# Performance work log

Measured on AMD Instinct MI355X. Metric: run time of the kernel, lower is better.

Reference implementation:

```python
import jax, jax.numpy as jnp
import numpy as np

NUM_HEADS = 16
DIM_EMBED = 1024
DIM_CROSS = 768
DIM_HEAD = DIM_EMBED // NUM_HEADS


def setup_inputs() -> dict:
    key = jax.random.key(0)
    ks = jax.random.split(key, 10)
    B, Sq, Skv = 16, 4096, 77
    s_e = 1.0 / np.sqrt(DIM_EMBED)
    s_c = 1.0 / np.sqrt(DIM_CROSS)
    return {
        "x": jax.random.normal(ks[0], (B, Sq, DIM_EMBED), jnp.float32),
        "y": jax.random.normal(ks[1], (B, Skv, DIM_CROSS), jnp.float32),
        "wq": jax.random.uniform(ks[2], (DIM_EMBED, DIM_EMBED), jnp.float32, -s_e, s_e),
        "bq": jax.random.uniform(ks[3], (DIM_EMBED,), jnp.float32, -s_e, s_e),
        "wk": jax.random.uniform(ks[4], (DIM_CROSS, DIM_EMBED), jnp.float32, -s_c, s_c),
        "bk": jax.random.uniform(ks[5], (DIM_EMBED,), jnp.float32, -s_c, s_c),
        "wv": jax.random.uniform(ks[6], (DIM_CROSS, DIM_EMBED), jnp.float32, -s_c, s_c),
        "bv": jax.random.uniform(ks[7], (DIM_EMBED,), jnp.float32, -s_c, s_c),
        "wo": jax.random.uniform(ks[8], (DIM_EMBED, DIM_EMBED), jnp.float32, -s_e, s_e),
        "bo": jax.random.uniform(ks[9], (DIM_EMBED,), jnp.float32, -s_e, s_e),
    }


def reference(x, y, wq, bq, wk, bk, wv, bv, wo, bo):
    B, Sq, E = x.shape
    H, D = NUM_HEADS, DIM_HEAD
    q = (x @ wq + bq).reshape(B, Sq, H, D).transpose(0, 2, 1, 3)   # [B,H,Sq,D]
    k = (y @ wk + bk).reshape(B, -1, H, D).transpose(0, 2, 1, 3)   # [B,H,Skv,D]
    v = (y @ wv + bv).reshape(B, -1, H, D).transpose(0, 2, 1, 3)   # [B,H,Skv,D]
    scale = 1.0 / jnp.sqrt(jnp.asarray(D, dtype=q.dtype))
    scores = jnp.einsum("bhqd,bhkd->bhqk", q, k) * scale           # [B,H,Sq,Skv]
    attn = jax.nn.softmax(scores, axis=-1)
    out = jnp.einsum("bhqk,bhkd->bhqd", attn, v)                   # [B,H,Sq,D]
    out = out.transpose(0, 2, 1, 3).reshape(B, Sq, E)
    return out @ wo + bo
```

## Files before the change

### kernel.cpp

```cpp
#include <hip/hip_runtime.h>

typedef unsigned short u16;
typedef __attribute__((ext_vector_type(4))) float f32x4;
typedef __attribute__((ext_vector_type(8))) short bf16x8;
typedef __attribute__((ext_vector_type(8))) unsigned short u16x8;
typedef __attribute__((ext_vector_type(4))) unsigned short u16x4;

__device__ __forceinline__ u16 f2bf(float f) {
  union { float f; unsigned u; } v; v.f = f;
  unsigned r = v.u + 0x7FFFu + ((v.u >> 16) & 1u);
  return (u16)(r >> 16);
}
__device__ __forceinline__ float bf2f(u16 h) {
  union { unsigned u; float f; } v; v.u = ((unsigned)h) << 16; return v.f;
}

__device__ __forceinline__ void gload_lds16(const void* g, void* l) {
  __builtin_amdgcn_global_load_lds((const __attribute__((address_space(1))) void*)g,
                                   (__attribute__((address_space(3))) void*)l, 16, 0, 0);
}


__global__ void k_zero(u16x8* __restrict__ p, int n8) {
  int i = blockIdx.x * blockDim.x + threadIdx.x;
  int stride = gridDim.x * blockDim.x;
  u16x8 z = (u16x8)0;
  for (; i < n8; i += stride) p[i] = z;
}

__global__ void k_cvt_x(const float* __restrict__ in, u16* __restrict__ out, int n4) {
  int i = blockIdx.x * blockDim.x + threadIdx.x;
  int stride = gridDim.x * blockDim.x;
  const f32x4* in4 = (const f32x4*)in;
  u16x4* out4 = (u16x4*)out;
  for (; i < n4; i += stride) {
    f32x4 v = in4[i];
    u16x4 o;
    o[0] = f2bf(v[0]); o[1] = f2bf(v[1]); o[2] = f2bf(v[2]); o[3] = f2bf(v[3]);
    out4[i] = o;
  }
}

__global__ void k_prep_wt(const float* __restrict__ wq, const float* __restrict__ wo,
                          const float* __restrict__ wk, const float* __restrict__ wv,
                          u16* __restrict__ WQ1T, u16* __restrict__ WO1T,
                          u16* __restrict__ WK1T, u16* __restrict__ WV1T) {
  __shared__ u16 tile[64][72];
  int bid = blockIdx.x;
  const float* w; u16* o; int K;
  if (bid < 256)      { w = wq; o = WQ1T; K = 1024; }
  else if (bid < 512) { w = wo; o = WO1T; K = 1024; bid -= 256; }
  else if (bid < 704) { w = wk; o = WK1T; K = 768;  bid -= 512; }
  else                { w = wv; o = WV1T; K = 768;  bid -= 704; }
  const int ti = bid >> 4, tj = bid & 15;
  const int t = threadIdx.x;
  const int r = t >> 2, cq = (t & 3) * 16;

  const float* src = w + (size_t)(ti * 64 + r) * 1024 + tj * 64 + cq;
#pragma unroll
  for (int j4 = 0; j4 < 4; ++j4) {
    f32x4 v = *(const f32x4*)(src + j4 * 4);
#pragma unroll
    for (int e = 0; e < 4; ++e) tile[r][cq + j4 * 4 + e] = f2bf(v[e]);
  }
  __syncthreads();

  u16 vals[16];
#pragma unroll
  for (int j = 0; j < 16; ++j) vals[j] = tile[cq + j][r];
  u16* dst = o + (size_t)(tj * 64 + r) * K + ti * 64 + cq;
  *(u16x8*)dst = *(u16x8*)&vals[0];
  *(u16x8*)(dst + 8) = *(u16x8*)&vals[8];
}

__global__ void k_prep_y(const float* __restrict__ y, u16* __restrict__ yb, int n4) {
  int i = blockIdx.x * blockDim.x + threadIdx.x;
  int stride = gridDim.x * blockDim.x;
  const f32x4* in4 = (const f32x4*)y;
  u16x4* out4 = (u16x4*)yb;
  for (; i < n4; i += stride) {
    f32x4 v = in4[i];
    u16x4 o;
    o[0] = f2bf(v[0]); o[1] = f2bf(v[1]); o[2] = f2bf(v[2]); o[3] = f2bf(v[3]);
    out4[i] = o;
  }
}

__global__ __launch_bounds__(256, 2) void k_gemm_kv(
    const u16* __restrict__ A,
    const u16* __restrict__ BK1, const float* __restrict__ bkb, u16* __restrict__ KTo,
    const u16* __restrict__ BV1, const float* __restrict__ bvb, u16* __restrict__ VTo)
{
  const int M = 1232, Kdim = 768;
  __shared__ u16 sA[128 * 32];
  __shared__ u16 sB[128 * 32];
  const int t = threadIdx.x;
  const int half = blockIdx.x >= 80;
  const int bb = blockIdx.x - half * 80;
  const u16* B = half ? BV1 : BK1;
  const float* bias = half ? bvb : bkb;
  u16* outp = half ? VTo : KTo;
  const int bm = bb / 8, bn = bb % 8;
  const int m0 = bm * 128, n0 = bn * 128;
  const int l = t & 63, wv_ = t >> 6;
  const int lr = l & 15, lg = l >> 4;
  const int wm = (wv_ >> 1) * 64, wn = (wv_ & 1) * 64;

  const int srow = t >> 2;
  const int ssw = ((t >> 2) & 3) ^ ((t >> 4) & 3);
  const int scol = ((t & 3) ^ ssw) * 8;
  char* ldsA = (char*)sA;
  char* ldsB = (char*)sB;
  const int ldsoff = wv_ * 1024;

  const int swl = (lr & 3) ^ ((lr >> 2) & 3);
  const int rds = (lg ^ swl) * 8;

  f32x4 acc[4][4] = {};

  for (int kt = 0; kt < Kdim / 32; ++kt) {
    const int k0 = kt * 32;
    __syncthreads();
    {
      int r1 = m0 + srow;       if (r1 > M - 1) r1 = M - 1;
      int r2 = m0 + 64 + srow;  if (r2 > M - 1) r2 = M - 1;
      gload_lds16(A + (size_t)r1 * Kdim + k0 + scol, ldsA + 0    + ldsoff);
      gload_lds16(A + (size_t)r2 * Kdim + k0 + scol, ldsA + 4096 + ldsoff);
      gload_lds16(B + (size_t)(n0 + srow) * Kdim + k0 + scol,      ldsB + 0    + ldsoff);
      gload_lds16(B + (size_t)(n0 + 64 + srow) * Kdim + k0 + scol, ldsB + 4096 + ldsoff);
    }
    __syncthreads();
    bf16x8 af[4], bfr[4];
#pragma unroll
    for (int mt = 0; mt < 4; ++mt)
      af[mt] = *(const bf16x8*)&sA[(wm + mt * 16 + lr) * 32 + rds];
#pragma unroll
    for (int nt = 0; nt < 4; ++nt)
      bfr[nt] = *(const bf16x8*)&sB[(wn + nt * 16 + lr) * 32 + rds];
#pragma unroll
    for (int mt = 0; mt < 4; ++mt)
#pragma unroll
      for (int nt = 0; nt < 4; ++nt)
        acc[mt][nt] = __builtin_amdgcn_mfma_f32_16x16x32_bf16(af[mt], bfr[nt], acc[mt][nt], 0, 0, 0);
  }

#pragma unroll
  for (int mt = 0; mt < 4; ++mt) {
#pragma unroll
    for (int nt = 0; nt < 4; ++nt) {
      const int gc = n0 + wn + nt * 16 + lr;
      const float bb2 = bias[gc];
#pragma unroll
      for (int r = 0; r < 4; ++r) {
        const int gr = m0 + wm + mt * 16 + lg * 4 + r;
        const float v = acc[mt][nt][r] + bb2;
        if (gr < M) {
          int bI = gr / 77, s = gr - bI * 77;
          int hh = gc >> 6, d = gc & 63;
          if (!half)
            outp[(((size_t)bI * 16 + hh) * 96 + s) * 64 + d] = f2bf(v);
          else
            outp[(((size_t)bI * 16 + hh) * 64 + d) * 96 + s] = f2bf(v);
        }
      }
    }
  }
}

template <int EPI>
__global__ __launch_bounds__(512, 2) void gemm8p(
    const u16* __restrict__ A, const u16* __restrict__ Bp,
    const float* __restrict__ bias, void* __restrict__ outp,
    const u16* __restrict__ KT, const u16* __restrict__ VT)
{
  __shared__ char lds[131072];
  const int t = threadIdx.x;
  const int cpx = (int)gridDim.x >> 3;
  const int swz = ((int)blockIdx.x & 7) * cpx + ((int)blockIdx.x >> 3);
  const int bm = swz >> 2, bn = swz & 3;
  const int m0 = bm * 256, n0 = bn * 256;
  const int w = t >> 6, l = t & 63, lr = l & 15, lg = l >> 4;
  const int wm = w >> 2, wn = w & 3;

  const int srow = t >> 3;
  const int scol = ((t & 7) ^ ((t >> 3) & 7)) << 3;
  const int sw0 = ((lg) ^ (lr & 7)) << 4;
  const int sw1 = ((4 + lg) ^ (lr & 7)) << 4;
  const int abase = wm * 128 + lr;
  const int bbase = wn * 64 + lr;

  f32x4 acc[8][4] = {};

#define RD_A(dst, db, mh, ksw) { _Pragma("unroll") for (int q = 0; q < 4; ++q) \
    dst[q] = *(const bf16x8*)(lds + (db) + ((abase + (mh) * 64 + q * 16) << 7) + (ksw)); }
#define RD_B(dst, db, ksw) { _Pragma("unroll") for (int nt = 0; nt < 4; ++nt) \
    dst[nt] = *(const bf16x8*)(lds + (db) + 32768 + ((bbase + nt * 16) << 7) + (ksw)); }
#define STG_A(kt, dn, j) gload_lds16(A + (size_t)(m0 + (j) * 64 + srow) * 1024 + (kt) * 64 + scol, \
                                     lds + (dn) + (j) * 8192 + t * 16)
#define STG_B(kt, dn, j) gload_lds16(Bp + (size_t)(n0 + (j) * 64 + srow) * 1024 + (kt) * 64 + scol, \
                                     lds + (dn) + 32768 + (j) * 8192 + t * 16)
#define MM16(ab, a_, b_) { __builtin_amdgcn_s_setprio(1); \
  _Pragma("unroll") for (int q = 0; q < 4; ++q) \
    _Pragma("unroll") for (int nt = 0; nt < 4; ++nt) \
      acc[(ab) + q][nt] = __builtin_amdgcn_mfma_f32_16x16x32_bf16(a_[q], b_[nt], acc[(ab) + q][nt], 0, 0, 0); \
  __builtin_amdgcn_s_setprio(0); }
#define BAR __builtin_amdgcn_s_barrier()
#define SB0 __builtin_amdgcn_sched_barrier(0)
#define VM2 asm volatile("s_waitcnt vmcnt(2)" ::: "memory")
#define VM4 asm volatile("s_waitcnt vmcnt(4)" ::: "memory")

  STG_B(0, 0, 0); STG_B(0, 0, 1);
  STG_A(0, 0, 0); STG_A(0, 0, 2);
  STG_B(0, 0, 2); STG_B(0, 0, 3);
  STG_A(0, 0, 1); STG_A(0, 0, 3);
  VM2; SB0; BAR;

#pragma unroll 2
  for (int c = 0; c < 16; ++c) {
    const int db = (c & 1) * 65536, dn = db ^ 65536;
    int cn = c + 1; if (cn > 15) cn = 15;
    bf16x8 a_[4], b0[4], b1[4];
    RD_A(a_, db, 0, sw0); RD_B(b0, db, sw0);
    STG_B(cn, dn, 0); STG_B(cn, dn, 1);
    BAR;
    MM16(0, a_, b0);
    BAR;
    RD_A(a_, db, 0, sw1); RD_B(b1, db, sw1);
    STG_A(cn, dn, 0); STG_A(cn, dn, 2);
    VM4; SB0; BAR;
    MM16(0, a_, b1);
    BAR;
    RD_A(a_, db, 1, sw0);
    STG_B(cn, dn, 2); STG_B(cn, dn, 3);
    BAR;
    MM16(4, a_, b0);
    BAR;
    RD_A(a_, db, 1, sw1);
    STG_A(cn, dn, 1); STG_A(cn, dn, 3);
    VM2; SB0; BAR;
    MM16(4, a_, b1);
    BAR;
  }
  asm volatile("s_waitcnt vmcnt(0)" ::: "memory");
  SB0; BAR;

#undef RD_A
#undef RD_B
#undef STG_A
#undef STG_B
#undef MM16
#undef BAR
#undef SB0
#undef VM2
#undef VM4

  if constexpr (EPI == 1) {
#pragma unroll
    for (int q = 0; q < 8; ++q) {
#pragma unroll
      for (int nt = 0; nt < 4; ++nt) {
        const int gc = n0 + wn * 64 + nt * 16 + lr;
        const float bb = bias[gc];
#pragma unroll
        for (int r = 0; r < 4; ++r) {
          const int gr = m0 + wm * 128 + q * 16 + lg * 4 + r;
          ((float*)outp)[(size_t)gr * 1024 + gc] = acc[q][nt][r] + bb;
        }
      }
    }
  } else {
    const int hh = (n0 >> 6) + wn;
    const int b = m0 >> 12;
    const u16* gK = KT + (size_t)(b * 16 + hh) * (96 * 64);
    const u16* gV = VT + (size_t)(b * 16 + hh) * (64 * 96);
    u16* Qs = (u16*)(lds + w * 16384);
    u16* Ps = (u16*)(lds + w * 16384 + 8192);
    u16* QBo = (u16*)outp;

    bf16x8 fk[5][2], fv[4][3];
#pragma unroll
    for (int nt = 0; nt < 5; ++nt)
#pragma unroll
      for (int ks = 0; ks < 2; ++ks)
        fk[nt][ks] = *(const bf16x8*)&gK[(nt * 16 + lr) * 64 + ks * 32 + lg * 8];
#pragma unroll
    for (int nt = 0; nt < 4; ++nt)
#pragma unroll
      for (int ks = 0; ks < 3; ++ks)
        fv[nt][ks] = *(const bf16x8*)&gV[(nt * 16 + lr) * 96 + ks * 32 + lg * 8];

    float bb[4];
#pragma unroll
    for (int nt = 0; nt < 4; ++nt) bb[nt] = bias[n0 + wn * 64 + nt * 16 + lr];

#pragma unroll
    for (int cc = 0; cc < 4; ++cc) {
#pragma unroll
      for (int qq = 0; qq < 2; ++qq)
#pragma unroll
        for (int nt = 0; nt < 4; ++nt)
#pragma unroll
          for (int r = 0; r < 4; ++r)
            Qs[(qq * 16 + lg * 4 + r) * 72 + nt * 16 + lr] =
                f2bf(acc[cc * 2 + qq][nt][r] + bb[nt]);

      bf16x8 aq[2][2];
#pragma unroll
      for (int qq = 0; qq < 2; ++qq)
#pragma unroll
        for (int ks = 0; ks < 2; ++ks)
          aq[qq][ks] = *(const bf16x8*)&Qs[(qq * 16 + lr) * 72 + ks * 32 + lg * 8];

      f32x4 s_[2][5] = {};
#pragma unroll
      for (int nt = 0; nt < 5; ++nt)
#pragma unroll
        for (int ks = 0; ks < 2; ++ks)
#pragma unroll
          for (int qq = 0; qq < 2; ++qq)
            s_[qq][nt] = __builtin_amdgcn_mfma_f32_16x16x32_bf16(aq[qq][ks], fk[nt][ks], s_[qq][nt], 0, 0, 0);
#pragma unroll
      for (int qq = 0; qq < 2; ++qq)
#pragma unroll
        for (int nt = 0; nt < 5; ++nt)
#pragma unroll
          for (int r = 0; r < 4; ++r)
            s_[qq][nt][r] *= 0.125f;
      if (lr >= 13) {
#pragma unroll
        for (int qq = 0; qq < 2; ++qq)
#pragma unroll
          for (int r = 0; r < 4; ++r)
            s_[qq][4][r] = -1e30f;
      }

      float ri[2][4];
#pragma unroll
      for (int qq = 0; qq < 2; ++qq) {
#pragma unroll
        for (int r = 0; r < 4; ++r) {
          float m1 = s_[qq][0][r];
#pragma unroll
          for (int nt = 1; nt < 5; ++nt) m1 = fmaxf(m1, s_[qq][nt][r]);
          m1 = fmaxf(m1, __shfl_xor(m1, 1, 64));
          m1 = fmaxf(m1, __shfl_xor(m1, 2, 64));
          m1 = fmaxf(m1, __shfl_xor(m1, 4, 64));
          m1 = fmaxf(m1, __shfl_xor(m1, 8, 64));
          float s1 = 0.f;
#pragma unroll
          for (int nt = 0; nt < 5; ++nt) {
            float e = __expf(s_[qq][nt][r] - m1);
            s_[qq][nt][r] = e;
            s1 += e;
          }
          s1 += __shfl_xor(s1, 1, 64);
          s1 += __shfl_xor(s1, 2, 64);
          s1 += __shfl_xor(s1, 4, 64);
          s1 += __shfl_xor(s1, 8, 64);
          ri[qq][r] = 1.0f / s1;
        }
      }

#pragma unroll
      for (int qq = 0; qq < 2; ++qq)
#pragma unroll
        for (int nt = 0; nt < 5; ++nt)
#pragma unroll
          for (int r = 0; r < 4; ++r)
            Ps[(qq * 16 + lg * 4 + r) * 104 + nt * 16 + lr] = f2bf(s_[qq][nt][r] * ri[qq][r]);
#pragma unroll
      for (int qq = 0; qq < 2; ++qq)
#pragma unroll
        for (int r = 0; r < 4; ++r)
          Ps[(qq * 16 + lg * 4 + r) * 104 + 80 + lr] = 0;

      f32x4 o_[2][4] = {};
#pragma unroll
      for (int ks = 0; ks < 3; ++ks) {
        bf16x8 ap[2];
#pragma unroll
        for (int qq = 0; qq < 2; ++qq)
          ap[qq] = *(const bf16x8*)&Ps[(qq * 16 + lr) * 104 + ks * 32 + lg * 8];
#pragma unroll
        for (int nt = 0; nt < 4; ++nt)
#pragma unroll
          for (int qq = 0; qq < 2; ++qq)
            o_[qq][nt] = __builtin_amdgcn_mfma_f32_16x16x32_bf16(ap[qq], fv[nt][ks], o_[qq][nt], 0, 0, 0);
      }

#pragma unroll
      for (int qq = 0; qq < 2; ++qq)
#pragma unroll
        for (int nt = 0; nt < 4; ++nt)
#pragma unroll
          for (int r = 0; r < 4; ++r)
            QBo[(size_t)(m0 + wm * 128 + cc * 32 + qq * 16 + lg * 4 + r) * 1024
                + hh * 64 + nt * 16 + lr] = f2bf(o_[qq][nt][r]);
    }
  }
}


extern "C" void kernel_launch(void* const* d_in, const int* in_sizes, int n_in,
                              void* d_out, int out_size, void* d_ws, size_t ws_size,
                              hipStream_t stream) {
  const float* x  = (const float*)d_in[0];
  const float* y  = (const float*)d_in[1];
  const float* wq = (const float*)d_in[2];
  const float* bq = (const float*)d_in[3];
  const float* wk = (const float*)d_in[4];
  const float* bk = (const float*)d_in[5];
  const float* wv = (const float*)d_in[6];
  const float* bv = (const float*)d_in[7];
  const float* wo = (const float*)d_in[8];
  const float* bo = (const float*)d_in[9];

  char* ws = (char*)d_ws;
  u16* QB   = (u16*)(ws + 0);
  u16* WQ1T = (u16*)(ws + 134217728);
  u16* WO1T = (u16*)(ws + 136314880);
  u16* WK1T = (u16*)(ws + 138412032);
  u16* WV1T = (u16*)(ws + 139984896);
  u16* YB   = (u16*)(ws + 141557760);
  u16* KT   = (u16*)(ws + 143654912);
  u16* VT   = (u16*)(ws + 146800640);

  u16*   XB  = (u16*)d_out;
  float* OUT = (float*)d_out;

  k_zero<<<768, 256, 0, stream>>>((u16x8*)KT, 393216);
  k_cvt_x<<<4096, 256, 0, stream>>>(x, XB, 16777216);
  k_prep_wt<<<896, 256, 0, stream>>>(wq, wo, wk, wv, WQ1T, WO1T, WK1T, WV1T);
  k_prep_y<<<924, 256, 0, stream>>>(y, YB, 236544);

  k_gemm_kv<<<160, 256, 0, stream>>>(YB, WK1T, bk, KT, WV1T, bv, VT);

  gemm8p<0><<<1024, 512, 0, stream>>>(XB, WQ1T, bq, QB, KT, VT);

  gemm8p<1><<<1024, 512, 0, stream>>>(QB, WO1T, bo, OUT, nullptr, nullptr);
}
```

Baseline: 490.3 us.

## Split output projection into dedicated kernel with 4-stage K=32 pipelined GEMM

The templated GEMM is split into two kernels: the Q-projection+attention kernel keeps the old main loop, while the output projection gets its own GEMM. The new one uses K-tiles of 32 with four LDS stages, a different XOR swizzle, and register double-buffered fragment reads. It uses s_setprio around the MFMA blocks and prefetches three stages ahead to hide global-load latency. The change is meant to improve load/compute overlap for the plain GEMM, at the cost of more barriers per K step and duplicated code.

```diff
diff --git a/kernel.cpp b/kernel.cpp
--- a/kernel.cpp
+++ b/kernel.cpp
@@ -167,10 +167,9 @@
   }
 }
 
-template <int EPI>
-__global__ __launch_bounds__(512, 2) void gemm8p(
+__global__ __launch_bounds__(512, 2) void k_qattn(
     const u16* __restrict__ A, const u16* __restrict__ Bp,
-    const float* __restrict__ bias, void* __restrict__ outp,
+    const float* __restrict__ bias, u16* __restrict__ QBo,
     const u16* __restrict__ KT, const u16* __restrict__ VT)
 {
   __shared__ char lds[131072];
@@ -254,148 +253,222 @@
 #undef VM2
 #undef VM4
 
-  if constexpr (EPI == 1) {
-#pragma unroll
-    for (int q = 0; q < 8; ++q) {
-#pragma unroll
-      for (int nt = 0; nt < 4; ++nt) {
-        const int gc = n0 + wn * 64 + nt * 16 + lr;
-        const float bb = bias[gc];
-#pragma unroll
-        for (int r = 0; r < 4; ++r) {
-          const int gr = m0 + wm * 128 + q * 16 + lg * 4 + r;
-          ((float*)outp)[(size_t)gr * 1024 + gc] = acc[q][nt][r] + bb;
+  const int hh = (n0 >> 6) + wn;
+  const int b = m0 >> 12;
+  const u16* gK = KT + (size_t)(b * 16 + hh) * (96 * 64);
+  const u16* gV = VT + (size_t)(b * 16 + hh) * (64 * 96);
+  u16* Qs = (u16*)(lds + w * 16384);
+  u16* Ps = (u16*)(lds + w * 16384 + 8192);
+
+  bf16x8 fk[5][2], fv[4][3];
+#pragma unroll
+  for (int nt = 0; nt < 5; ++nt)
+#pragma unroll
+    for (int ks = 0; ks < 2; ++ks)
+      fk[nt][ks] = *(const bf16x8*)&gK[(nt * 16 + lr) * 64 + ks * 32 + lg * 8];
+#pragma unroll
+  for (int nt = 0; nt < 4; ++nt)
+#pragma unroll
+    for (int ks = 0; ks < 3; ++ks)
+      fv[nt][ks] = *(const bf16x8*)&gV[(nt * 16 + lr) * 96 + ks * 32 + lg * 8];
+
+  float bb[4];
+#pragma unroll
+  for (int nt = 0; nt < 4; ++nt) bb[nt] = bias[n0 + wn * 64 + nt * 16 + lr];
+
+#pragma unroll
+  for (int cc = 0; cc < 4; ++cc) {
+#pragma unroll
+    for (int qq = 0; qq < 2; ++qq)
+#pragma unroll
+      for (int nt = 0; nt < 4; ++nt)
+#pragma unroll
+        for (int r = 0; r < 4; ++r)
+          Qs[(qq * 16 + lg * 4 + r) * 72 + nt * 16 + lr] =
+              f2bf(acc[cc * 2 + qq][nt][r] + bb[nt]);
+
+    bf16x8 aq[2][2];
+#pragma unroll
+    for (int qq = 0; qq < 2; ++qq)
+#pragma unroll
+      for (int ks = 0; ks < 2; ++ks)
+        aq[qq][ks] = *(const bf16x8*)&Qs[(qq * 16 + lr) * 72 + ks * 32 + lg * 8];
+
+    f32x4 s_[2][5] = {};
+#pragma unroll
+    for (int nt = 0; nt < 5; ++nt)
+#pragma unroll
+      for (int ks = 0; ks < 2; ++ks)
+#pragma unroll
+        for (int qq = 0; qq < 2; ++qq)
+          s_[qq][nt] = __builtin_amdgcn_mfma_f32_16x16x32_bf16(aq[qq][ks], fk[nt][ks], s_[qq][nt], 0, 0, 0);
+#pragma unroll
+    for (int qq = 0; qq < 2; ++qq)
+#pragma unroll
+      for (int nt = 0; nt < 5; ++nt)
+#pragma unroll
+        for (int r = 0; r < 4; ++r)
+          s_[qq][nt][r] *= 0.125f;
+    if (lr >= 13) {
+#pragma unroll
+      for (int qq = 0; qq < 2; ++qq)
+#pragma unroll
+        for (int r = 0; r < 4; ++r)
+          s_[qq][4][r] = -1e30f;
+    }
+
+    float ri[2][4];
+#pragma unroll
+    for (int qq = 0; qq < 2; ++qq) {
+#pragma unroll
+      for (int r = 0; r < 4; ++r) {
+        float m1 = s_[qq][0][r];
+#pragma unroll
+        for (int nt = 1; nt < 5; ++nt) m1 = fmaxf(m1, s_[qq][nt][r]);
+        m1 = fmaxf(m1, __shfl_xor(m1, 1, 64));
+        m1 = fmaxf(m1, __shfl_xor(m1, 2, 64));
+        m1 = fmaxf(m1, __shfl_xor(m1, 4, 64));
+        m1 = fmaxf(m1, __shfl_xor(m1, 8, 64));
+        float s1 = 0.f;
+#pragma unroll
+        for (int nt = 0; nt < 5; ++nt) {
+          float e = __expf(s_[qq][nt][r] - m1);
+          s_[qq][nt][r] = e;
+          s1 += e;
         }
+        s1 += __shfl_xor(s1, 1, 64);
+        s1 += __shfl_xor(s1, 2, 64);
+        s1 += __shfl_xor(s1, 4, 64);
+        s1 += __shfl_xor(s1, 8, 64);
+        ri[qq][r] = 1.0f / s1;
       }
     }
-  } else {
-    const int hh = (n0 >> 6) + wn;
-    const int b = m0 >> 12;
-    const u16* gK = KT + (size_t)(b * 16 + hh) * (96 * 64);
-    const u16* gV = VT + (size_t)(b * 16 + hh) * (64 * 96);
-    u16* Qs = (u16*)(lds + w * 16384);
-    u16* Ps = (u16*)(lds + w * 16384 + 8192);
-    u16* QBo = (u16*)outp;
-
-    bf16x8 fk[5][2], fv[4][3];
-#pragma unroll
-    for (int nt = 0; nt < 5; ++nt)
-#pragma unroll
-      for (int ks = 0; ks < 2; ++ks)
-        fk[nt][ks] = *(const bf16x8*)&gK[(nt * 16 + lr) * 64 + ks * 32 + lg * 8];
-#pragma unroll
-    for (int nt = 0; nt < 4; ++nt)
-#pragma unroll
-      for (int ks = 0; ks < 3; ++ks)
-        fv[nt][ks] = *(const bf16x8*)&gV[(nt * 16 + lr) * 96 + ks * 32 + lg * 8];
-
-    float bb[4];
-#pragma unroll
-    for (int nt = 0; nt < 4; ++nt) bb[nt] = bias[n0 + wn * 64 + nt * 16 + lr];
-
-#pragma unroll
-    for (int cc = 0; cc < 4; ++cc) {
+
+#pragma unroll
+    for (int qq = 0; qq < 2; ++qq)
+#pragma unroll
+      for (int nt = 0; nt < 5; ++nt)
+#pragma unroll
+        for (int r = 0; r < 4; ++r)
+          Ps[(qq * 16 + lg * 4 + r) * 104 + nt * 16 + lr] = f2bf(s_[qq][nt][r] * ri[qq][r]);
+#pragma unroll
+    for (int qq = 0; qq < 2; ++qq)
+#pragma unroll
+      for (int r = 0; r < 4; ++r)
+        Ps[(qq * 16 + lg * 4 + r) * 104 + 80 + lr] = 0;
+
+    f32x4 o_[2][4] = {};
+#pragma unroll
+    for (int ks = 0; ks < 3; ++ks) {
+      bf16x8 ap[2];
 #pragma unroll
       for (int qq = 0; qq < 2; ++qq)
-#pragma unroll
-        for (int nt = 0; nt < 4; ++nt)
-#pragma unroll
-          for (int r = 0; r < 4; ++r)
-            Qs[(qq * 16 + lg * 4 + r) * 72 + nt * 16 + lr] =
-                f2bf(acc[cc * 2 + qq][nt][r] + bb[nt]);
-
-      bf16x8 aq[2][2];
-#pragma unroll
-      for (int qq = 0; qq < 2; ++qq)
-#pragma unroll
-        for (int ks = 0; ks < 2; ++ks)
-          aq[qq][ks] = *(const bf16x8*)&Qs[(qq * 16 + lr) * 72 + ks * 32 + lg * 8];
-
-      f32x4 s_[2][5] = {};
-#pragma unroll
-      for (int nt = 0; nt < 5; ++nt)
-#pragma unroll
-        for (int ks = 0; ks < 2; ++ks)
-#pragma unroll
-          for (int qq = 0; qq < 2; ++qq)
-            s_[qq][nt] = __builtin_amdgcn_mfma_f32_16x16x32_bf16(aq[qq][ks], fk[nt][ks], s_[qq][nt], 0, 0, 0);
-#pragma unroll
-      for (int qq = 0; qq < 2; ++qq)
-#pragma unroll
-        for (int nt = 0; nt < 5; ++nt)
-#pragma unroll
-          for (int r = 0; r < 4; ++r)
-            s_[qq][nt][r] *= 0.125f;
-      if (lr >= 13) {
+        ap[qq] = *(const bf16x8*)&Ps[(qq * 16 + lr) * 104 + ks * 32 + lg * 8];
+#pragma unroll
+      for (int nt = 0; nt < 4; ++nt)
 #pragma unroll
         for (int qq = 0; qq < 2; ++qq)
-#pragma unroll
-          for (int r = 0; r < 4; ++r)
-            s_[qq][4][r] = -1e30f;
+          o_[qq][nt] = __builtin_amdgcn_mfma_f32_16x16x32_bf16(ap[qq], fv[nt][ks], o_[qq][nt], 0, 0, 0);
+    }
+
+#pragma unroll
+    for (int qq = 0; qq < 2; ++qq)
+#pragma unroll
+      for (int nt = 0; nt < 4; ++nt)
+#pragma unroll
+        for (int r = 0; r < 4; ++r)
+          QBo[(size_t)(m0 + wm * 128 + cc * 32 + qq * 16 + lg * 4 + r) * 1024
+              + hh * 64 + nt * 16 + lr] = f2bf(o_[qq][nt][r]);
+  }
+}
+
+__global__ __launch_bounds__(512, 2) void k_oproj(
+    const u16* __restrict__ A, const u16* __restrict__ Bp,
+    const float* __restrict__ bias, float* __restrict__ outp)
+{
+  __shared__ char lds[131072];
+  const int t = threadIdx.x;
+  const int cpx = (int)gridDim.x >> 3;
+  const int swz = ((int)blockIdx.x & 7) * cpx + ((int)blockIdx.x >> 3);
+  const int bm = swz >> 2, bn = swz & 3;
+  const int m0 = bm * 256, n0 = bn * 256;
+  const int w = t >> 6, l = t & 63, lr = l & 15, lg = l >> 4;
+  const int wm = w >> 2, wn = w & 3;
+
+  const int srow = t >> 2;
+  const int scol = ((t & 3) ^ ((t >> 2) & 3) ^ ((t >> 4) & 3)) * 8;
+  const int rsw = (lg ^ (lr & 3) ^ ((lr >> 2) & 3)) << 4;
+  const int arow = wm * 128 + lr;
+  const int brow = wn * 64 + lr;
+
+  f32x4 acc[8][4] = {};
+
+#define RD(dstA, dstB, sbb) { \
+  _Pragma("unroll") for (int q = 0; q < 8; ++q) \
+    dstA[q] = *(const bf16x8*)(lds + (sbb) + ((arow + q * 16) << 6) + rsw); \
+  _Pragma("unroll") for (int nt = 0; nt < 4; ++nt) \
+    dstB[nt] = *(const bf16x8*)(lds + (sbb) + 16384 + ((brow + nt * 16) << 6) + rsw); }
+#define STAGE(kt, sbb) { \
+    gload_lds16(A  + (size_t)(m0 + srow) * 1024 + (kt) * 32 + scol,       lds + (sbb) + t * 16); \
+    gload_lds16(A  + (size_t)(m0 + 128 + srow) * 1024 + (kt) * 32 + scol, lds + (sbb) + 8192 + t * 16); \
+    gload_lds16(Bp + (size_t)(n0 + srow) * 1024 + (kt) * 32 + scol,       lds + (sbb) + 16384 + t * 16); \
+    gload_lds16(Bp + (size_t)(n0 + 128 + srow) * 1024 + (kt) * 32 + scol, lds + (sbb) + 24576 + t * 16); }
+#define MM(a_, b_) { __builtin_amdgcn_s_setprio(1); \
+  _Pragma("unroll") for (int q = 0; q < 8; ++q) \
+    _Pragma("unroll") for (int nt = 0; nt < 4; ++nt) \
+      acc[q][nt] = __builtin_amdgcn_mfma_f32_16x16x32_bf16(a_[q], b_[nt], acc[q][nt], 0, 0, 0); \
+  __builtin_amdgcn_s_setprio(0); }
+#define BAR __builtin_amdgcn_s_barrier()
+#define SB0 __builtin_amdgcn_sched_barrier(0)
+#define VM8 asm volatile("s_waitcnt vmcnt(8)" ::: "memory")
+
+  bf16x8 aA[8], bA[4], aB[8], bB[4];
+
+  STAGE(0, 0); STAGE(1, 32768); STAGE(2, 65536);
+  VM8; SB0; BAR;
+  RD(aA, bA, 0);
+
+  int rdo = 32768, sto = 98304;
+#pragma unroll 1
+  for (int tt = 0; tt < 32; tt += 2) {
+    {
+      int ks = tt + 3; if (ks > 31) ks = 31;
+      STAGE(ks, sto); sto = (sto + 32768) & 131071;
+      VM8; SB0; BAR;
+      RD(aB, bB, rdo); rdo = (rdo + 32768) & 131071;
+      MM(aA, bA);
+      BAR;
+    }
+    {
+      int ks = tt + 4; if (ks > 31) ks = 31;
+      STAGE(ks, sto); sto = (sto + 32768) & 131071;
+      VM8; SB0; BAR;
+      RD(aA, bA, rdo); rdo = (rdo + 32768) & 131071;
+      MM(aB, bB);
+      BAR;
+    }
+  }
+  asm volatile("s_waitcnt vmcnt(0)" ::: "memory");
+  SB0;
+
+#undef RD
+#undef STAGE
+#undef MM
+#undef BAR
+#undef SB0
+#undef VM8
+
+#pragma unroll
+  for (int q = 0; q < 8; ++q) {
+#pragma unroll
+    for (int nt = 0; nt < 4; ++nt) {
+      const int gc = n0 + wn * 64 + nt * 16 + lr;
+      const float bb = bias[gc];
+#pragma unroll
+      for (int r = 0; r < 4; ++r) {
+        const int gr = m0 + wm * 128 + q * 16 + lg * 4 + r;
+        outp[(size_t)gr * 1024 + gc] = acc[q][nt][r] + bb;
       }
-
-      float ri[2][4];
-#pragma unroll
-      for (int qq = 0; qq < 2; ++qq) {
-#pragma unroll
-        for (int r = 0; r < 4; ++r) {
-          float m1 = s_[qq][0][r];
-#pragma unroll
-          for (int nt = 1; nt < 5; ++nt) m1 = fmaxf(m1, s_[qq][nt][r]);
-          m1 = fmaxf(m1, __shfl_xor(m1, 1, 64));
-          m1 = fmaxf(m1, __shfl_xor(m1, 2, 64));
-          m1 = fmaxf(m1, __shfl_xor(m1, 4, 64));
-          m1 = fmaxf(m1, __shfl_xor(m1, 8, 64));
-          float s1 = 0.f;
-#pragma unroll
-          for (int nt = 0; nt < 5; ++nt) {
-            float e = __expf(s_[qq][nt][r] - m1);
-            s_[qq][nt][r] = e;
-            s1 += e;
-          }
-          s1 += __shfl_xor(s1, 1, 64);
-          s1 += __shfl_xor(s1, 2, 64);
-          s1 += __shfl_xor(s1, 4, 64);
-          s1 += __shfl_xor(s1, 8, 64);
-          ri[qq][r] = 1.0f / s1;
-        }
-      }
-
-#pragma unroll
-      for (int qq = 0; qq < 2; ++qq)
-#pragma unroll
-        for (int nt = 0; nt < 5; ++nt)
-#pragma unroll
-          for (int r = 0; r < 4; ++r)
-            Ps[(qq * 16 + lg * 4 + r) * 104 + nt * 16 + lr] = f2bf(s_[qq][nt][r] * ri[qq][r]);
-#pragma unroll
-      for (int qq = 0; qq < 2; ++qq)
-#pragma unroll
-        for (int r = 0; r < 4; ++r)
-          Ps[(qq * 16 + lg * 4 + r) * 104 + 80 + lr] = 0;
-
-      f32x4 o_[2][4] = {};
-#pragma unroll
-      for (int ks = 0; ks < 3; ++ks) {
-        bf16x8 ap[2];
-#pragma unroll
-        for (int qq = 0; qq < 2; ++qq)
-          ap[qq] = *(const bf16x8*)&Ps[(qq * 16 + lr) * 104 + ks * 32 + lg * 8];
-#pragma unroll
-        for (int nt = 0; nt < 4; ++nt)
-#pragma unroll
-          for (int qq = 0; qq < 2; ++qq)
-            o_[qq][nt] = __builtin_amdgcn_mfma_f32_16x16x32_bf16(ap[qq], fv[nt][ks], o_[qq][nt], 0, 0, 0);
-      }
-
-#pragma unroll
-      for (int qq = 0; qq < 2; ++qq)
-#pragma unroll
-        for (int nt = 0; nt < 4; ++nt)
-#pragma unroll
-          for (int r = 0; r < 4; ++r)
-            QBo[(size_t)(m0 + wm * 128 + cc * 32 + qq * 16 + lg * 4 + r) * 1024
-                + hh * 64 + nt * 16 + lr] = f2bf(o_[qq][nt][r]);
     }
   }
 }
@@ -435,7 +508,7 @@
 
   k_gemm_kv<<<160, 256, 0, stream>>>(YB, WK1T, bk, KT, WV1T, bv, VT);
 
-  gemm8p<0><<<1024, 512, 0, stream>>>(XB, WQ1T, bq, QB, KT, VT);
-
-  gemm8p<1><<<1024, 512, 0, stream>>>(QB, WO1T, bo, OUT, nullptr, nullptr);
-}
+  k_qattn<<<1024, 512, 0, stream>>>(XB, WQ1T, bq, QB, KT, VT);
+
+  k_oproj<<<1024, 512, 0, stream>>>(QB, WO1T, bo, OUT);
+}
```

Result: slower. 508.5 us (+3.7%).

## Restructure GEMM main loop into two phases with fewer barriers

Applied to the files above, without the earlier changes.

The bf16 MFMA GEMM inner loop is reorganized from four barrier-separated sub-steps into two phases. Each phase loads both K-halves of the A fragments (and both B halves up front), issues more global-to-LDS prefetches at once, then runs two MFMA groups back-to-back. This is meant to cut s_barrier count and give longer uninterrupted MFMA runs for latency hiding. In exchange it uses more registers for the extra fragment arrays, which may reduce occupancy, and the wait counts change (vmcnt 6 and vmcnt 2).

```diff
diff --git a/kernel.cpp b/kernel.cpp
--- a/kernel.cpp
+++ b/kernel.cpp
@@ -207,11 +207,10 @@
 #define BAR __builtin_amdgcn_s_barrier()
 #define SB0 __builtin_amdgcn_sched_barrier(0)
 #define VM2 asm volatile("s_waitcnt vmcnt(2)" ::: "memory")
-#define VM4 asm volatile("s_waitcnt vmcnt(4)" ::: "memory")
-
-  STG_B(0, 0, 0); STG_B(0, 0, 1);
+#define VM6 asm volatile("s_waitcnt vmcnt(6)" ::: "memory")
+
+  STG_B(0, 0, 0); STG_B(0, 0, 1); STG_B(0, 0, 2); STG_B(0, 0, 3);
   STG_A(0, 0, 0); STG_A(0, 0, 2);
-  STG_B(0, 0, 2); STG_B(0, 0, 3);
   STG_A(0, 0, 1); STG_A(0, 0, 3);
   VM2; SB0; BAR;
 
@@ -219,27 +218,19 @@
   for (int c = 0; c < 16; ++c) {
     const int db = (c & 1) * 65536, dn = db ^ 65536;
     int cn = c + 1; if (cn > 15) cn = 15;
-    bf16x8 a_[4], b0[4], b1[4];
-    RD_A(a_, db, 0, sw0); RD_B(b0, db, sw0);
-    STG_B(cn, dn, 0); STG_B(cn, dn, 1);
-    BAR;
-    MM16(0, a_, b0);
-    BAR;
-    RD_A(a_, db, 0, sw1); RD_B(b1, db, sw1);
+    bf16x8 a0_[4], a1_[4], b0[4], b1[4];
+    RD_A(a0_, db, 0, sw0); RD_A(a1_, db, 0, sw1);
+    RD_B(b0, db, sw0); RD_B(b1, db, sw1);
+    STG_B(cn, dn, 0); STG_B(cn, dn, 1); STG_B(cn, dn, 2); STG_B(cn, dn, 3);
     STG_A(cn, dn, 0); STG_A(cn, dn, 2);
-    VM4; SB0; BAR;
-    MM16(0, a_, b1);
-    BAR;
-    RD_A(a_, db, 1, sw0);
-    STG_B(cn, dn, 2); STG_B(cn, dn, 3);
-    BAR;
-    MM16(4, a_, b0);
-    BAR;
-    RD_A(a_, db, 1, sw1);
+    MM16(0, a0_, b0);
+    MM16(0, a1_, b1);
+    VM6; SB0; BAR;
+    RD_A(a0_, db, 1, sw0); RD_A(a1_, db, 1, sw1);
     STG_A(cn, dn, 1); STG_A(cn, dn, 3);
+    MM16(4, a0_, b0);
+    MM16(4, a1_, b1);
     VM2; SB0; BAR;
-    MM16(4, a_, b1);
-    BAR;
   }
   asm volatile("s_waitcnt vmcnt(0)" ::: "memory");
   SB0; BAR;
@@ -252,7 +243,7 @@
 #undef BAR
 #undef SB0
 #undef VM2
-#undef VM4
+#undef VM6
 
   if constexpr (EPI == 1) {
 #pragma unroll
```

New measurement: 486.4 us. Within noise of the previous version (-0.8%).
